# Performance work log

Measured on AMD Instinct MI355X. Metric: run time of the kernel, lower is better.

## Reference

```python
import jax, jax.numpy as jnp
import numpy as np

EPS_LOG = 1e-08   # module eps (added inside log)
EPS_PD = 1e-06    # torch.nn.PairwiseDistance default eps (added to the difference)


def setup_inputs() -> dict:
    key = jax.random.key(0)
    x = jax.random.normal(key, (8192, 512), dtype=jnp.float32)
    return {"x": x}


def reference(x) -> jnp.ndarray:
    n = x.shape[0]
    # Cosine/dot similarity matrix [n, n]; mask the diagonal with -1 so a
    # point cannot be its own nearest neighbor.
    dots = x @ x.T
    idx = jnp.arange(n)
    dots = dots.at[idx, idx].set(-1.0)
    # Nearest neighbor (by dot product) per row; indices — no gradient path.
    I = jnp.argmax(dots, axis=1)
    # PairwiseDistance(p=2): ||x - x[I] + eps||_2 per row.
    diff = x - x[I] + EPS_PD
    rho = jnp.sqrt(jnp.sum(diff * diff, axis=1))
    loss = -jnp.mean(jnp.log(rho + EPS_LOG))
    return loss
```

## Files before the change

kernel.cpp:

```cpp
#include <hip/hip_runtime.h>


#define NPTS 8192
#define DIM  512
#define BM   128
#define BN   128
#define NTIL 64
#define NBLK (NTIL * (NTIL + 1) / 2)
#define KT_N 8

typedef float f32x4 __attribute__((ext_vector_type(4)));
typedef long  lx2   __attribute__((ext_vector_type(2)));

__device__ __forceinline__ unsigned char f32_to_e4m3(float f) {
  unsigned u = __builtin_bit_cast(unsigned, f);
  unsigned s = (u >> 24) & 0x80u;
  unsigned a = u & 0x7FFFFFFFu;
  float af = __builtin_bit_cast(float, a);
  if (af < 0.015625f) {
    int m = (int)rintf(af * 512.0f);
    return (unsigned char)(s | (unsigned)m);
  }
  unsigned u2 = a + 0x0007FFFFu + ((a >> 20) & 1u);
  int e = (int)(u2 >> 23) - 127 + 7;
  unsigned m = (u2 >> 20) & 7u;
  if (e > 15) return (unsigned char)(s | 0x7Eu);
  return (unsigned char)(s | ((unsigned)e << 3) | m);
}

__device__ __forceinline__ unsigned int mono_f32(float f) {
  unsigned u = __builtin_bit_cast(unsigned, f);
  return u ^ (0x80000000u | (unsigned)((int)u >> 31));
}

__global__ void cvt_fp8_kernel(const float* __restrict__ x,
                               unsigned char* __restrict__ xq,
                               unsigned long long* __restrict__ nn64) {
  int i = blockIdx.x * blockDim.x + threadIdx.x;
  const float4* xp = reinterpret_cast<const float4*>(x) + 2 * (size_t)i;
  float4 v0 = xp[0], v1 = xp[1];
  unsigned long long w =
      (unsigned long long)f32_to_e4m3(v0.x) |
      ((unsigned long long)f32_to_e4m3(v0.y) << 8) |
      ((unsigned long long)f32_to_e4m3(v0.z) << 16) |
      ((unsigned long long)f32_to_e4m3(v0.w) << 24) |
      ((unsigned long long)f32_to_e4m3(v1.x) << 32) |
      ((unsigned long long)f32_to_e4m3(v1.y) << 40) |
      ((unsigned long long)f32_to_e4m3(v1.z) << 48) |
      ((unsigned long long)f32_to_e4m3(v1.w) << 56);
  reinterpret_cast<unsigned long long*>(xq)[i] = w;
  if (i < NPTS) nn64[i] = 0ull;
}

__device__ __forceinline__ void gload_lds16(const unsigned char* g,
                                            unsigned char* l) {
  __builtin_amdgcn_global_load_lds(
      (__attribute__((address_space(1))) const void*)g,
      (__attribute__((address_space(3))) void*)l, 16, 0, 0);
}

__device__ __forceinline__ unsigned long long kmax(unsigned long long a,
                                                   unsigned long long b) {
  return a > b ? a : b;
}

__global__ __launch_bounds__(256, 3) void tri_gemm_kernel(
    const unsigned char* __restrict__ xq,
    unsigned long long* __restrict__ nn64) {
  __shared__ unsigned char lds[3][16384];

  const int orig = (int)blockIdx.x;
  int b = (orig & 7) * (NBLK >> 3) + (orig >> 3);
  int ti = (int)((sqrtf(8.0f * (float)b + 1.0f) - 1.0f) * 0.5f);
  while ((ti + 1) * (ti + 2) / 2 <= b) ++ti;
  while (ti * (ti + 1) / 2 > b) --ti;
  const int tj = b - ti * (ti + 1) / 2;

  const int tid  = (int)threadIdx.x;
  const int wid  = tid >> 6;
  const int lane = tid & 63;
  const int wr   = wid >> 1;
  const int wc   = wid & 1;
  const int l15  = lane & 15;
  const int l16  = lane >> 4;
  const int arow0 = ti * BM;
  const int bcol0 = tj * BN;

#define STAGE(bufi, kt) do {                                                 \
    _Pragma("unroll")                                                        \
    for (int i_ = 0; i_ < 2; ++i_) {                                         \
      const int chunk_ = (i_ << 8) + tid;                        \
      const int row_   = chunk_ >> 2;                            \
      const int c_     = ((chunk_ & 3) - ((row_ >> 1) & 3)) & 3;             \
      gload_lds16(xq + (size_t)(arow0 + row_) * DIM + (kt) * 64 + (c_ << 4), \
                  &lds[bufi][chunk_ << 4]);                                   \
      gload_lds16(xq + (size_t)(bcol0 + row_) * DIM + (kt) * 64 + (c_ << 4), \
                  &lds[bufi][8192 + (chunk_ << 4)]);                          \
    }                                                                        \
  } while (0)

  const int rot = (l15 >> 1) & 3;
  int aoff[4], boff[4];
#pragma unroll
  for (int mi = 0; mi < 4; ++mi)
    aoff[mi] = (wr * 64 + mi * 16 + l15) * 64 + (((l16 + rot) & 3) << 4);
#pragma unroll
  for (int ni = 0; ni < 4; ++ni)
    boff[ni] = 8192 + (wc * 64 + ni * 16 + l15) * 64 + (((l16 + rot) & 3) << 4);

  f32x4 acc[4][4];
#pragma unroll
  for (int mi = 0; mi < 4; ++mi)
#pragma unroll
    for (int ni = 0; ni < 4; ++ni)
      acc[mi][ni] = (f32x4){0.f, 0.f, 0.f, 0.f};

  STAGE(0, 0);
  STAGE(1, 1);

  for (int u = 0; u < KT_N; ++u) {
    const int cur = u - (u / 3) * 3;
    if (u == KT_N - 1) {
      asm volatile("s_waitcnt vmcnt(0)" ::: "memory");
    } else {
      asm volatile("s_waitcnt vmcnt(4)" ::: "memory");
    }
    asm volatile("s_barrier" ::: "memory");
    if (u + 2 < KT_N) {
      const int nb = (u + 2) - ((u + 2) / 3) * 3;
      STAGE(nb, u + 2);
    }

    lx2 a2[4], b2[4];
#pragma unroll
    for (int mi = 0; mi < 4; ++mi)
      a2[mi] = *reinterpret_cast<const lx2*>(&lds[cur][aoff[mi]]);
#pragma unroll
    for (int ni = 0; ni < 4; ++ni)
      b2[ni] = *reinterpret_cast<const lx2*>(&lds[cur][boff[ni]]);
    __builtin_amdgcn_s_setprio(1);
#pragma unroll
    for (int mi = 0; mi < 4; ++mi)
#pragma unroll
      for (int ni = 0; ni < 4; ++ni) {
        acc[mi][ni] = __builtin_amdgcn_mfma_f32_16x16x32_fp8_fp8(
            a2[mi][0], b2[ni][0], acc[mi][ni], 0, 0, 0);
        acc[mi][ni] = __builtin_amdgcn_mfma_f32_16x16x32_fp8_fp8(
            a2[mi][1], b2[ni][1], acc[mi][ni], 0, 0, 0);
      }
    __builtin_amdgcn_s_setprio(0);
  }
#undef STAGE

  const bool diagw = (ti == tj) && (wr == wc);

  unsigned long long K[16];
  const unsigned jb = ~(unsigned)(bcol0 + wc * 64 + l15);
#pragma unroll
  for (int mi = 0; mi < 4; ++mi)
#pragma unroll
    for (int j = 0; j < 4; ++j) {
      unsigned long long best = 0ull;
#pragma unroll
      for (int ni = 0; ni < 4; ++ni) {
        unsigned long long kk =
            ((unsigned long long)mono_f32(acc[mi][ni][j]) << 32) |
            (unsigned)(jb - ni * 16);
        if (diagw && mi == ni && (l16 * 4 + j) == l15) kk = 0ull;
        best = kmax(best, kk);
      }
      K[mi * 4 + j] = best;
    }
#pragma unroll
  for (int k = 0; k < 4; ++k) {
    const int m = 1 << k;
    const unsigned kb = (unsigned)(l15 >> k) & 1u;
#pragma unroll
    for (int i = 0; i < (8 >> k); ++i) {
      unsigned long long lo = K[2 * i], hi = K[2 * i + 1];
      unsigned long long keep = kb ? hi : lo;
      unsigned long long send = kb ? lo : hi;
      unsigned long long recv =
          (unsigned long long)__shfl_xor((long long)send, m);
      K[i] = kmax(keep, recv);
    }
  }
  {
    const int gi = arow0 + wr * 64 + (l15 >> 2) * 16 + l16 * 4 + (l15 & 3);
    atomicMax(&nn64[gi], K[0]);
  }

  unsigned long long C[4];
  const unsigned ib = ~(unsigned)(arow0 + wr * 64 + l16 * 4);
#pragma unroll
  for (int ni = 0; ni < 4; ++ni) {
    unsigned long long best = 0ull;
#pragma unroll
    for (int mi = 0; mi < 4; ++mi)
#pragma unroll
      for (int j = 0; j < 4; ++j) {
        unsigned long long kk =
            ((unsigned long long)mono_f32(acc[mi][ni][j]) << 32) |
            (unsigned)(ib - (mi * 16 + j));
        if (diagw && mi == ni && (l16 * 4 + j) == l15) kk = 0ull;
        best = kmax(best, kk);
      }
    C[ni] = best;
  }
#pragma unroll
  for (int k = 0; k < 2; ++k) {
    const int m = 16 << k;
    const unsigned kb = (unsigned)(lane >> (4 + k)) & 1u;
#pragma unroll
    for (int i = 0; i < (2 >> k); ++i) {
      unsigned long long lo = C[2 * i], hi = C[2 * i + 1];
      unsigned long long keep = kb ? hi : lo;
      unsigned long long send = kb ? lo : hi;
      unsigned long long recv =
          (unsigned long long)__shfl_xor((long long)send, m);
      C[i] = kmax(keep, recv);
    }
  }
  {
    const int gj = bcol0 + wc * 64 + l16 * 16 + l15;
    atomicMax(&nn64[gj], C[0]);
  }
}

__global__ void dist_log_kernel(const float* __restrict__ x,
                                const unsigned long long* __restrict__ nn64,
                                float* __restrict__ logs) {
  const int row  = blockIdx.x * 4 + ((int)threadIdx.x >> 6);
  const int lane = (int)threadIdx.x & 63;
  const int nn   = (int)(~(unsigned int)(nn64[row] & 0xFFFFFFFFull)) & (NPTS - 1);
  const float4* xr = reinterpret_cast<const float4*>(x + (size_t)row * DIM);
  const float4* xn = reinterpret_cast<const float4*>(x + (size_t)nn  * DIM);
  float s = 0.f;
#pragma unroll
  for (int i = 0; i < 2; ++i) {
    float4 a = xr[lane + i * 64];
    float4 b = xn[lane + i * 64];
    float d0 = a.x - b.x + 1e-6f;
    float d1 = a.y - b.y + 1e-6f;
    float d2 = a.z - b.z + 1e-6f;
    float d3 = a.w - b.w + 1e-6f;
    s += d0 * d0 + d1 * d1 + d2 * d2 + d3 * d3;
  }
#pragma unroll
  for (int m = 32; m >= 1; m >>= 1) s += __shfl_xor(s, m);
  if (lane == 0) logs[row] = logf(sqrtf(s) + 1e-8f);
}

__global__ void final_reduce_kernel(const float* __restrict__ logs,
                                    float* __restrict__ out) {
  __shared__ float sm[1024];
  const int t = (int)threadIdx.x;
  float s = 0.f;
#pragma unroll
  for (int i = 0; i < 8; ++i) s += logs[t * 8 + i];
  sm[t] = s;
  __syncthreads();
  for (int k = 512; k > 0; k >>= 1) {
    if (t < k) sm[t] += sm[t + k];
    __syncthreads();
  }
  if (t == 0) out[0] = -(sm[0] / (float)NPTS);
}

extern "C" void kernel_launch(void* const* d_in, const int* in_sizes, int n_in,
                              void* d_out, int out_size, void* d_ws, size_t ws_size,
                              hipStream_t stream) {
  const float* x = (const float*)d_in[0];
  float* out = (float*)d_out;
  char* ws = (char*)d_ws;

  unsigned char*      xq   = (unsigned char*)(ws);
  unsigned long long* nn64 = (unsigned long long*)(ws + 4194304);
  float*              logs = (float*)(ws + 4259840);

  cvt_fp8_kernel<<<(NPTS * DIM / 8) / 256, 256, 0, stream>>>(x, xq, nn64);

  tri_gemm_kernel<<<NBLK, 256, 0, stream>>>(xq, nn64);

  dist_log_kernel<<<NPTS / 4, 256, 0, stream>>>(x, nn64, logs);

  final_reduce_kernel<<<1, 1024, 0, stream>>>(logs, out);
}
```

Before: 49.70 us.

## Switch FP8 GEMM to 32x32x64 scaled MFMA with new LDS swizzle and reductions

Replaces the 16x16x32 fp8 MFMA tiles (4x4 per wave, two instructions per k-step) with 2x2 tiles of the gfx950 mfma_scale 32x32x64 f8f6f4 instruction, using neutral scales. The LDS swizzle and per-lane read offsets are reworked to fit the 32-lane fragment layout, with two 16-byte reads per operand. The argmax epilogue is rewritten for the 32x32 accumulator layout, adding a longer row shuffle tree and a simpler column reduction. The goal is fewer MFMA issues and fewer LDS reads per k-step; the risks are index-mapping errors and heavier register use from 32-entry key arrays.

Result: no change. 50.17 us (+0.9%).

```diff
diff --git a/kernel.cpp b/kernel.cpp
--- a/kernel.cpp
+++ b/kernel.cpp
@@ -9,8 +9,9 @@
 #define NBLK (NTIL * (NTIL + 1) / 2)
 #define KT_N 8
 
-typedef float f32x4 __attribute__((ext_vector_type(4)));
-typedef long  lx2   __attribute__((ext_vector_type(2)));
+typedef float f32x16 __attribute__((ext_vector_type(16)));
+typedef int   i32x4  __attribute__((ext_vector_type(4)));
+typedef int   i32x8  __attribute__((ext_vector_type(8)));
 
 __device__ __forceinline__ unsigned char f32_to_e4m3(float f) {
   unsigned u = __builtin_bit_cast(unsigned, f);
@@ -81,8 +82,8 @@
   const int lane = tid & 63;
   const int wr   = wid >> 1;
   const int wc   = wid & 1;
-  const int l15  = lane & 15;
-  const int l16  = lane >> 4;
+  const int l31  = lane & 31;
+  const int h    = lane >> 5;
   const int arow0 = ti * BM;
   const int bcol0 = tj * BN;
 
@@ -91,7 +92,8 @@
     for (int i_ = 0; i_ < 2; ++i_) {                                         \
       const int chunk_ = (i_ << 8) + tid;                        \
       const int row_   = chunk_ >> 2;                            \
-      const int c_     = ((chunk_ & 3) - ((row_ >> 1) & 3)) & 3;             \
+      const int f_     = ((row_ >> 1) + (row_ >> 3)) & 3;                    \
+      const int c_     = ((chunk_ & 3) - f_) & 3;                            \
       gload_lds16(xq + (size_t)(arow0 + row_) * DIM + (kt) * 64 + (c_ << 4), \
                   &lds[bufi][chunk_ << 4]);                                   \
       gload_lds16(xq + (size_t)(bcol0 + row_) * DIM + (kt) * 64 + (c_ << 4), \
@@ -99,21 +101,21 @@
     }                                                                        \
   } while (0)
 
-  const int rot = (l15 >> 1) & 3;
-  int aoff[4], boff[4];
-#pragma unroll
-  for (int mi = 0; mi < 4; ++mi)
-    aoff[mi] = (wr * 64 + mi * 16 + l15) * 64 + (((l16 + rot) & 3) << 4);
-#pragma unroll
-  for (int ni = 0; ni < 4; ++ni)
-    boff[ni] = 8192 + (wc * 64 + ni * 16 + l15) * 64 + (((l16 + rot) & 3) << 4);
-
-  f32x4 acc[4][4];
-#pragma unroll
-  for (int mi = 0; mi < 4; ++mi)
-#pragma unroll
-    for (int ni = 0; ni < 4; ++ni)
-      acc[mi][ni] = (f32x4){0.f, 0.f, 0.f, 0.f};
+  const int fr  = ((l31 >> 1) + (l31 >> 3)) & 3;
+  const int s0  = (2 * h + fr) & 3;
+  const int s1  = (2 * h + 1 + fr) & 3;
+  const int abase = (wr * 64 + l31) * 64;
+  const int bbase = 8192 + (wc * 64 + l31) * 64;
+  const int aoff0 = abase + (s0 << 4), aoff1 = abase + (s1 << 4);
+  const int boff0 = bbase + (s0 << 4), boff1 = bbase + (s1 << 4);
+
+  f32x16 acc[2][2];
+#pragma unroll
+  for (int mi = 0; mi < 2; ++mi)
+#pragma unroll
+    for (int ni = 0; ni < 2; ++ni)
+#pragma unroll
+      for (int r = 0; r < 16; ++r) acc[mi][ni][r] = 0.f;
 
   STAGE(0, 0);
   STAGE(1, 1);
@@ -131,52 +133,57 @@
       STAGE(nb, u + 2);
     }
 
-    lx2 a2[4], b2[4];
-#pragma unroll
-    for (int mi = 0; mi < 4; ++mi)
-      a2[mi] = *reinterpret_cast<const lx2*>(&lds[cur][aoff[mi]]);
-#pragma unroll
-    for (int ni = 0; ni < 4; ++ni)
-      b2[ni] = *reinterpret_cast<const lx2*>(&lds[cur][boff[ni]]);
+    i32x8 a8[2], b8[2];
+#pragma unroll
+    for (int mi = 0; mi < 2; ++mi) {
+      i32x4 lo = *reinterpret_cast<const i32x4*>(&lds[cur][aoff0 + mi * 2048]);
+      i32x4 hi = *reinterpret_cast<const i32x4*>(&lds[cur][aoff1 + mi * 2048]);
+      a8[mi] = (i32x8){lo[0], lo[1], lo[2], lo[3], hi[0], hi[1], hi[2], hi[3]};
+    }
+#pragma unroll
+    for (int ni = 0; ni < 2; ++ni) {
+      i32x4 lo = *reinterpret_cast<const i32x4*>(&lds[cur][boff0 + ni * 2048]);
+      i32x4 hi = *reinterpret_cast<const i32x4*>(&lds[cur][boff1 + ni * 2048]);
+      b8[ni] = (i32x8){lo[0], lo[1], lo[2], lo[3], hi[0], hi[1], hi[2], hi[3]};
+    }
     __builtin_amdgcn_s_setprio(1);
 #pragma unroll
-    for (int mi = 0; mi < 4; ++mi)
-#pragma unroll
-      for (int ni = 0; ni < 4; ++ni) {
-        acc[mi][ni] = __builtin_amdgcn_mfma_f32_16x16x32_fp8_fp8(
-            a2[mi][0], b2[ni][0], acc[mi][ni], 0, 0, 0);
-        acc[mi][ni] = __builtin_amdgcn_mfma_f32_16x16x32_fp8_fp8(
-            a2[mi][1], b2[ni][1], acc[mi][ni], 0, 0, 0);
-      }
+    for (int mi = 0; mi < 2; ++mi)
+#pragma unroll
+      for (int ni = 0; ni < 2; ++ni)
+        acc[mi][ni] = __builtin_amdgcn_mfma_scale_f32_32x32x64_f8f6f4(
+            a8[mi], b8[ni], acc[mi][ni], 0, 0,
+            0, 0x7F7F7F7F, 0, 0x7F7F7F7F);
     __builtin_amdgcn_s_setprio(0);
   }
 #undef STAGE
 
   const bool diagw = (ti == tj) && (wr == wc);
 
-  unsigned long long K[16];
-  const unsigned jb = ~(unsigned)(bcol0 + wc * 64 + l15);
-#pragma unroll
-  for (int mi = 0; mi < 4; ++mi)
-#pragma unroll
-    for (int j = 0; j < 4; ++j) {
+  unsigned long long K[32];
+  const unsigned jb = ~(unsigned)(bcol0 + wc * 64 + l31);
+#pragma unroll
+  for (int mi = 0; mi < 2; ++mi)
+#pragma unroll
+    for (int r = 0; r < 16; ++r) {
+      const int rl = (r & 3) + 8 * (r >> 2) + 4 * h;
       unsigned long long best = 0ull;
 #pragma unroll
-      for (int ni = 0; ni < 4; ++ni) {
+      for (int ni = 0; ni < 2; ++ni) {
         unsigned long long kk =
-            ((unsigned long long)mono_f32(acc[mi][ni][j]) << 32) |
-            (unsigned)(jb - ni * 16);
-        if (diagw && mi == ni && (l16 * 4 + j) == l15) kk = 0ull;
+            ((unsigned long long)mono_f32(acc[mi][ni][r]) << 32) |
+            (unsigned)(jb - ni * 32);
+        if (diagw && mi == ni && rl == l31) kk = 0ull;
         best = kmax(best, kk);
       }
-      K[mi * 4 + j] = best;
-    }
-#pragma unroll
-  for (int k = 0; k < 4; ++k) {
+      K[mi * 16 + r] = best;
+    }
+#pragma unroll
+  for (int k = 0; k < 5; ++k) {
     const int m = 1 << k;
-    const unsigned kb = (unsigned)(l15 >> k) & 1u;
-#pragma unroll
-    for (int i = 0; i < (8 >> k); ++i) {
+    const unsigned kb = (unsigned)(lane >> k) & 1u;
+#pragma unroll
+    for (int i = 0; i < (16 >> k); ++i) {
       unsigned long long lo = K[2 * i], hi = K[2 * i + 1];
       unsigned long long keep = kb ? hi : lo;
       unsigned long long send = kb ? lo : hi;
@@ -186,44 +193,37 @@
     }
   }
   {
-    const int gi = arow0 + wr * 64 + (l15 >> 2) * 16 + l16 * 4 + (l15 & 3);
+    const int s = l31;
+    const int gi = arow0 + wr * 64 + (s >> 4) * 32 +
+                   ((s & 3) + 8 * ((s & 15) >> 2) + 4 * h);
     atomicMax(&nn64[gi], K[0]);
   }
 
-  unsigned long long C[4];
-  const unsigned ib = ~(unsigned)(arow0 + wr * 64 + l16 * 4);
-#pragma unroll
-  for (int ni = 0; ni < 4; ++ni) {
-    unsigned long long best = 0ull;
-#pragma unroll
-    for (int mi = 0; mi < 4; ++mi)
-#pragma unroll
-      for (int j = 0; j < 4; ++j) {
-        unsigned long long kk =
-            ((unsigned long long)mono_f32(acc[mi][ni][j]) << 32) |
-            (unsigned)(ib - (mi * 16 + j));
-        if (diagw && mi == ni && (l16 * 4 + j) == l15) kk = 0ull;
-        best = kmax(best, kk);
+  {
+    unsigned long long C0 = 0ull, C1 = 0ull;
+    const unsigned ib = ~(unsigned)(arow0 + wr * 64);
+#pragma unroll
+    for (int mi = 0; mi < 2; ++mi)
+#pragma unroll
+      for (int r = 0; r < 16; ++r) {
+        const int rl = (r & 3) + 8 * (r >> 2) + 4 * h;
+        const unsigned idxk = (unsigned)(ib - (mi * 32 + rl));
+        unsigned long long k0 =
+            ((unsigned long long)mono_f32(acc[mi][0][r]) << 32) | idxk;
+        if (diagw && mi == 0 && rl == l31) k0 = 0ull;
+        C0 = kmax(C0, k0);
+        unsigned long long k1 =
+            ((unsigned long long)mono_f32(acc[mi][1][r]) << 32) | idxk;
+        if (diagw && mi == 1 && rl == l31) k1 = 0ull;
+        C1 = kmax(C1, k1);
       }
-    C[ni] = best;
-  }
-#pragma unroll
-  for (int k = 0; k < 2; ++k) {
-    const int m = 16 << k;
-    const unsigned kb = (unsigned)(lane >> (4 + k)) & 1u;
-#pragma unroll
-    for (int i = 0; i < (2 >> k); ++i) {
-      unsigned long long lo = C[2 * i], hi = C[2 * i + 1];
-      unsigned long long keep = kb ? hi : lo;
-      unsigned long long send = kb ? lo : hi;
-      unsigned long long recv =
-          (unsigned long long)__shfl_xor((long long)send, m);
-      C[i] = kmax(keep, recv);
-    }
-  }
-  {
-    const int gj = bcol0 + wc * 64 + l16 * 16 + l15;
-    atomicMax(&nn64[gj], C[0]);
+    unsigned long long keep = h ? C1 : C0;
+    unsigned long long send = h ? C0 : C1;
+    unsigned long long recv =
+        (unsigned long long)__shfl_xor((long long)send, 32);
+    unsigned long long R = kmax(keep, recv);
+    const int gj = bcol0 + wc * 64 + h * 32 + l31;
+    atomicMax(&nn64[gj], R);
   }
 }
 
```
